# Optimization experiments

Hardware: AMD Instinct MI355X
Metric: run time of the kernel (lower is better)

## Reference

```python
import jax, jax.numpy as jnp
import numpy as np
from jax import lax

L, B, N, D = 6, 4, 2048, 512
H, DH = 8, 64
ID = H * DH           # 512
M = 266               # int(64*log(64)) random features
INNER = 2 * D         # conformer expansion
K = 31                # depthwise kernel
PAD = (15, 15)        # calc_same_padding(31)
EPS_LN = 1e-5


def setup_inputs() -> dict:
    key = jax.random.key(0)
    ks = jax.random.split(key, 12)
    s = 0.02
    return {
        "x": jax.random.normal(ks[0], (B, N, D), jnp.float32),
        "ln1_g": jnp.ones((L, D), jnp.float32),
        "ln1_b": jnp.zeros((L, D), jnp.float32),
        "wq": jax.random.normal(ks[1], (L, ID, D), jnp.float32) * s,
        "bq": jnp.zeros((L, ID), jnp.float32),
        "wk": jax.random.normal(ks[2], (L, ID, D), jnp.float32) * s,
        "bk": jnp.zeros((L, ID), jnp.float32),
        "wv": jax.random.normal(ks[3], (L, ID, D), jnp.float32) * s,
        "bv": jnp.zeros((L, ID), jnp.float32),
        "wo": jax.random.normal(ks[4], (L, ID, D), jnp.float32) * s,
        "bo": jnp.zeros((L, D), jnp.float32),
        # FAVOR+ random projection buffer (gaussian orthogonal ~ iid gaussian rows)
        "proj": jax.random.normal(ks[5], (L, M, DH), jnp.float32),
        "ln2_g": jnp.ones((L, D), jnp.float32),
        "ln2_b": jnp.zeros((L, D), jnp.float32),
        "pw1_w": jax.random.normal(ks[6], (L, 2 * INNER, D), jnp.float32) * s,
        "pw1_b": jnp.zeros((L, 2 * INNER), jnp.float32),
        "dw_w": jax.random.normal(ks[7], (L, INNER, K), jnp.float32) * s,
        "dw_b": jnp.zeros((L, INNER), jnp.float32),
        "pw2_w": jax.random.normal(ks[8], (L, D, INNER), jnp.float32) * s,
        "pw2_b": jnp.zeros((L, D), jnp.float32),
    }


def layer_norm(x, g, b):
    mu = jnp.mean(x, axis=-1, keepdims=True)
    var = jnp.mean((x - mu) ** 2, axis=-1, keepdims=True)
    return (x - mu) * lax.rsqrt(var + EPS_LN) * g + b


def softmax_kernel(data, proj, is_query, eps=1e-4):
    # data: [b,h,n,dh], proj: [m,dh]
    dn = DH ** -0.25
    ratio = M ** -0.5
    data_dash = jnp.einsum('bhnd,md->bhnm', dn * data, proj)
    diag = jnp.sum(data * data, axis=-1, keepdims=True) * 0.5 * dn * dn  # [b,h,n,1]
    if is_query:
        mx = jnp.max(data_dash, axis=-1, keepdims=True)
        return ratio * (jnp.exp(data_dash - diag - mx) + eps)
    else:
        return ratio * jnp.exp(data_dash - diag + eps)


def favor_attention(q, k, v, proj):
    qp = softmax_kernel(q, proj, True)   # [b,h,n,m]
    kp = softmax_kernel(k, proj, False)  # [b,h,n,m]
    k_cumsum = jnp.sum(kp, axis=-2)      # [b,h,m]
    d_inv = 1.0 / (jnp.einsum('bhnm,bhm->bhn', qp, k_cumsum) + 1e-8)
    context = jnp.einsum('bhnm,bhne->bhme', kp, v)          # [b,h,m,dh]
    out = jnp.einsum('bhme,bhnm,bhn->bhne', context, qp, d_inv)
    return out


def pcmer_forward(x, ln1_g, ln1_b, wq, bq, wk, bk, wv, bv, wo, bo, proj,
                  ln2_g, ln2_b, pw1_w, pw1_b, dw_w, dw_b, pw2_w, pw2_b):
    for l in range(L):
        # --- self attention (FAVOR+) ---
        h = layer_norm(x, ln1_g[l], ln1_b[l])
        q = (h @ wq[l].T + bq[l]).reshape(B, N, H, DH).transpose(0, 2, 1, 3)
        k = (h @ wk[l].T + bk[l]).reshape(B, N, H, DH).transpose(0, 2, 1, 3)
        v = (h @ wv[l].T + bv[l]).reshape(B, N, H, DH).transpose(0, 2, 1, 3)
        o = favor_attention(q, k, v, proj[l])                 # [b,h,n,dh]
        o = o.transpose(0, 2, 1, 3).reshape(B, N, ID)
        x = x + (o @ wo[l].T + bo[l])
        # --- conformer conv module ---
        h = layer_norm(x, ln2_g[l], ln2_b[l])
        y = h @ pw1_w[l].T + pw1_b[l]                         # [b,n,2*inner]
        a, g = y[..., :INNER], y[..., INNER:]
        y = a * jax.nn.sigmoid(g)                             # GLU
        yt = jnp.pad(y.transpose(0, 2, 1), ((0, 0), (0, 0), PAD))  # [b,inner,n+30]
        dw = lax.conv_general_dilated(
            yt, dw_w[l][:, None, :], window_strides=(1,), padding='VALID',
            feature_group_count=INNER,
            dimension_numbers=('NCH', 'OIH', 'NCH')) + dw_b[l][None, :, None]
        dw = jax.nn.silu(dw).transpose(0, 2, 1)               # [b,n,inner]
        x = x + (dw @ pw2_w[l].T + pw2_b[l])
    return x


def reference(x, ln1_g, ln1_b, wq, bq, wk, bk, wv, bv, wo, bo, proj,
              ln2_g, ln2_b, pw1_w, pw1_b, dw_w, dw_b, pw2_w, pw2_b):
    return pcmer_forward(x, ln1_g, ln1_b, wq, bq, wk, bk, wv, bv, wo, bo, proj,
                         ln2_g, ln2_b, pw1_w, pw1_b, dw_w, dw_b, pw2_w, pw2_b)
```

## Files before the change

### kernel.cpp

```cpp
#include <hip/hip_runtime.h>


#define L_LAYERS 6
#define B_ 4
#define N_ 2048
#define D_ 512
#define H_ 8
#define DH_ 64
#define M_ 266
#define INNER_ 1024
#define T_ 8192
#define PS_ 320
#define QKVS_ 1536
#define NS_ 8

typedef __attribute__((ext_vector_type(8))) short short8;
typedef __attribute__((ext_vector_type(4))) float floatx4;

__device__ __forceinline__ ushort f2bf(float f) {
  union { float f; uint u; } v; v.f = f;
  uint r = v.u + 0x7fffu + ((v.u >> 16) & 1u);
  return (ushort)(r >> 16);
}
__device__ __forceinline__ float bf2f(ushort u) {
  union { uint u; float f; } v; v.u = ((uint)u) << 16;
  return v.f;
}
__device__ __forceinline__ float wave_sum(float v) {
#pragma unroll
  for (int m = 1; m < 64; m <<= 1) v += __shfl_xor(v, m);
  return v;
}
__device__ __forceinline__ void async_cp16(const void* g, void* l) {
  __builtin_amdgcn_global_load_lds(
      (const __attribute__((address_space(1))) void*)g,
      (__attribute__((address_space(3))) void*)l, 16, 0, 0);
}
__device__ __forceinline__ int xcd_swz(int bid, int n) {
  return (bid & 7) * (n >> 3) + (bid >> 3);
}

__global__ void f2bf4_dual(const float4* __restrict__ s1, int n1,
                           const float4* __restrict__ s2, int n2,
                           ushort* __restrict__ out) {
  int i = blockIdx.x * 256 + threadIdx.x;
  if (i >= n1 + n2) return;
  float4 v = (i < n1) ? s1[i] : s2[i - n1];
  ushort4 r;
  r.x = f2bf(v.x); r.y = f2bf(v.y); r.z = f2bf(v.z); r.w = f2bf(v.w);
  *(ushort4*)(out + (size_t)i * 4) = r;
}
__global__ void pack_qkv_w3(const float4* __restrict__ wq, const float4* __restrict__ wk,
                            const float4* __restrict__ wv, ushort* __restrict__ dst) {
  int i = blockIdx.x * 256 + threadIdx.x;
  const int per = L_LAYERS * 512 * 128;
  if (i >= 3 * per) return;
  int seg = i / per;
  int rem = i - seg * per;
  const float4* src = seg == 0 ? wq : (seg == 1 ? wk : wv);
  int l = rem >> 16;
  int r2 = rem & 65535;
  int row = r2 >> 7, c4 = r2 & 127;
  float4 v = src[rem];
  ushort4 r;
  r.x = f2bf(v.x); r.y = f2bf(v.y); r.z = f2bf(v.z); r.w = f2bf(v.w);
  *(ushort4*)(dst + ((size_t)l * QKVS_ + seg * 512 + row) * 512 + c4 * 4) = r;
}
__global__ void pack_small(const float* __restrict__ bq, const float* __restrict__ bk,
                           const float* __restrict__ bv, float* __restrict__ bqkv,
                           const float* __restrict__ proj, ushort* __restrict__ pjp,
                           const float* __restrict__ pw1b, float* __restrict__ pb1) {
  int i = blockIdx.x * 256 + threadIdx.x;
  const int A = L_LAYERS * QKVS_;
  const int Bn = L_LAYERS * 320 * 64;
  const int C = L_LAYERS * 2048;
  if (i < A) {
    int l = i / QKVS_, c = i % QKVS_;
    bqkv[i] = c < 512 ? bq[l * 512 + c]
                      : (c < 1024 ? bk[l * 512 + c - 512] : bv[l * 512 + c - 1024]);
  } else if (i < A + Bn) {
    int j = i - A;
    int l = j / (320 * 64), rem = j % (320 * 64), m = rem >> 6, kk = rem & 63;
    pjp[j] = (m < M_) ? f2bf(proj[((size_t)l * M_ + m) * 64 + kk]) : (ushort)0;
  } else if (i < A + Bn + C) {
    int j = i - A - Bn;
    int l = j >> 11, cp = j & 2047;
    int s = (cp >> 4) & 1;
    int srow = ((cp >> 5) << 4) + (cp & 15) + s * 1024;
    pb1[j] = pw1b[l * 2048 + srow];
  }
}
__global__ void pack_pw1_w(const float4* __restrict__ src, ushort* __restrict__ dst) {
  int i = blockIdx.x * 256 + threadIdx.x;
  if (i >= L_LAYERS * 2048 * 128) return;
  int l = i >> 18;
  int rem = i & 262143;
  int cp = rem >> 7, c4 = rem & 127;
  int s = (cp >> 4) & 1;
  int srow = ((cp >> 5) << 4) + (cp & 15) + s * 1024;
  float4 v = src[((size_t)l * 2048 + srow) * 128 + c4];
  ushort4 r;
  r.x = f2bf(v.x); r.y = f2bf(v.y); r.z = f2bf(v.z); r.w = f2bf(v.w);
  *(ushort4*)(dst + ((size_t)l * 2048 + cp) * 512 + c4 * 4) = r;
}

__global__ __launch_bounds__(256) void ln_kernel(const float* __restrict__ x,
                                                 const float* __restrict__ g,
                                                 const float* __restrict__ b,
                                                 ushort* __restrict__ out) {
  const int t = blockIdx.x;
  const int tid = threadIdx.x;
  const float* row = x + (size_t)t * D_;
  float v0 = row[tid], v1 = row[tid + 256];
  float s1 = v0 + v1;
  float s2 = v0 * v0 + v1 * v1;
  s1 = wave_sum(s1);
  s2 = wave_sum(s2);
  __shared__ float sh1[4], sh2[4];
  int w = tid >> 6;
  if ((tid & 63) == 0) { sh1[w] = s1; sh2[w] = s2; }
  __syncthreads();
  s1 = sh1[0] + sh1[1] + sh1[2] + sh1[3];
  s2 = sh2[0] + sh2[1] + sh2[2] + sh2[3];
  float mu = s1 * (1.f / D_);
  float var = s2 * (1.f / D_) - mu * mu;
  float rs = rsqrtf(var + 1e-5f);
  out[(size_t)t * D_ + tid]       = f2bf((v0 - mu) * rs * g[tid] + b[tid]);
  out[(size_t)t * D_ + tid + 256] = f2bf((v1 - mu) * rs * g[tid + 256] + b[tid + 256]);
}

template <bool OUT_BF16, int ACT, int KT>
__global__ __launch_bounds__(256, 2) void gemm_big(const ushort* __restrict__ A,
                                                   const ushort* __restrict__ W,
                                                   const float* __restrict__ bias,
                                                   void* __restrict__ Cout,
                                                   int ldc) {
  constexpr int NT = KT / 32;
  __shared__ ushort As[3][256 * 32];
  __shared__ ushort Bs[3][128 * 32];
  const int tid = threadIdx.x;
  const int w = tid >> 6, lane = tid & 63;
  const int row0 = xcd_swz(blockIdx.x, gridDim.x) * 256, col0 = blockIdx.y * 128;
  const int rl = lane >> 2;
  const int lc = ((lane & 3) ^ ((lane >> 3) & 3)) * 8;
  const ushort* gA = A + (size_t)(row0 + w * 64 + rl) * KT + lc;
  const ushort* gB = W + (size_t)(col0 + w * 32 + rl) * KT + lc;
  const int m16 = lane & 15, quad = lane >> 4;
  const int awr = (w >> 1) * 128;
  const int bwc = (w & 1) * 64;
  floatx4 acc[8][4] = {};

  auto stage = [&](int t, int buf) {
#pragma unroll
    for (int j = 0; j < 4; j++)
      async_cp16(gA + ((size_t)j * 16) * KT + t * 32, As[buf] + w * 2048 + j * 512);
#pragma unroll
    for (int j = 0; j < 2; j++)
      async_cp16(gB + ((size_t)j * 16) * KT + t * 32, Bs[buf] + w * 1024 + j * 512);
  };
  auto body = [&](int buf, bool bar2) {
    short8 af[8], bfr[4];
#pragma unroll
    for (int i = 0; i < 8; i++) {
      int r = awr + i * 16 + m16;
      af[i] = *(const short8*)&As[buf][r * 32 + (quad ^ ((r >> 1) & 3)) * 8];
    }
#pragma unroll
    for (int j = 0; j < 4; j++) {
      int r = bwc + j * 16 + m16;
      bfr[j] = *(const short8*)&Bs[buf][r * 32 + (quad ^ ((r >> 1) & 3)) * 8];
    }
    if (bar2) {
      asm volatile("s_waitcnt lgkmcnt(0)" ::: "memory");
      __builtin_amdgcn_sched_barrier(0);
      __builtin_amdgcn_s_barrier();
    }
    __builtin_amdgcn_s_setprio(1);
#pragma unroll
    for (int i = 0; i < 8; i++)
#pragma unroll
      for (int j = 0; j < 4; j++)
        acc[i][j] = __builtin_amdgcn_mfma_f32_16x16x32_bf16(af[i], bfr[j], acc[i][j], 0, 0, 0);
    __builtin_amdgcn_s_setprio(0);
  };

  stage(0, 0);
  stage(1, 1);
  int c = 0;
  for (int t = 0; t < NT - 2; t++) {
    int pf = c + 2; if (pf >= 3) pf -= 3;
    stage(t + 2, pf);
    asm volatile("s_waitcnt vmcnt(12)" ::: "memory");
    __builtin_amdgcn_s_barrier();
    body(c, true);
    c++; if (c >= 3) c -= 3;
  }
  asm volatile("s_waitcnt vmcnt(6)" ::: "memory");
  __builtin_amdgcn_s_barrier();
  body(c, false);
  c++; if (c >= 3) c -= 3;
  asm volatile("s_waitcnt vmcnt(0)" ::: "memory");
  __builtin_amdgcn_s_barrier();
  body(c, false);

  if (ACT == 0) {
#pragma unroll
    for (int i = 0; i < 8; i++) {
      const int r0 = row0 + awr + i * 16 + quad * 4;
#pragma unroll
      for (int j = 0; j < 4; j++) {
        const int cc = col0 + bwc + j * 16 + m16;
        const float bv = bias[cc];
#pragma unroll
        for (int r = 0; r < 4; r++) {
          float vv = acc[i][j][r] + bv;
          if (OUT_BF16) ((ushort*)Cout)[(size_t)(r0 + r) * ldc + cc] = f2bf(vv);
          else          ((float*)Cout)[(size_t)(r0 + r) * ldc + cc] = vv;
        }
      }
    }
  } else {
#pragma unroll
    for (int i = 0; i < 8; i++) {
      const int r0 = row0 + awr + i * 16 + quad * 4;
#pragma unroll
      for (int jp = 0; jp < 2; jp++) {
        const int j = jp * 2;
        const int ca = col0 + bwc + j * 16 + m16;
        const float ba = bias[ca], bg = bias[ca + 16];
        const int oc = ((col0 + bwc) >> 1) + jp * 16 + m16;
#pragma unroll
        for (int r = 0; r < 4; r++) {
          float a = acc[i][j][r] + ba;
          float g = acc[i][j + 1][r] + bg;
          float z = a / (1.f + expf(-g));
          ((ushort*)Cout)[(size_t)(r0 + r) * ldc + oc] = f2bf(z);
        }
      }
    }
  }
}

template <int KT>
__global__ __launch_bounds__(256, 4) void gemm_small(const ushort* __restrict__ A,
                                                     const ushort* __restrict__ W,
                                                     const float* __restrict__ bias,
                                                     const float* __restrict__ res,
                                                     float* __restrict__ Cout,
                                                     int ldc) {
  constexpr int NT = KT / 32;
  __shared__ ushort As[3][64 * 32];
  __shared__ ushort Bs[3][128 * 32];
  const int tid = threadIdx.x;
  const int w = tid >> 6, lane = tid & 63;
  const int row0 = xcd_swz(blockIdx.x, gridDim.x) * 64, col0 = blockIdx.y * 128;
  const int rl = lane >> 2;
  const int lc = ((lane & 3) ^ ((lane >> 3) & 3)) * 8;
  const ushort* gA = A + (size_t)(row0 + w * 16 + rl) * KT + lc;
  const ushort* gB0 = W + (size_t)(col0 + w * 32 + rl) * KT + lc;
  const ushort* gB1 = gB0 + (size_t)16 * KT;
  const int m16 = lane & 15, quad = lane >> 4;
  const int awr = (w >> 1) * 32;
  const int bwc = (w & 1) * 64;
  floatx4 acc[2][4] = {};

  auto stage = [&](int t, int buf) {
    async_cp16(gA + t * 32, As[buf] + w * 512);
    async_cp16(gB0 + t * 32, Bs[buf] + w * 1024);
    async_cp16(gB1 + t * 32, Bs[buf] + w * 1024 + 512);
  };
  auto body = [&](int buf, bool bar2) {
    short8 af[2], bfr[4];
#pragma unroll
    for (int i = 0; i < 2; i++) {
      int r = awr + i * 16 + m16;
      af[i] = *(const short8*)&As[buf][r * 32 + (quad ^ ((r >> 1) & 3)) * 8];
    }
#pragma unroll
    for (int j = 0; j < 4; j++) {
      int r = bwc + j * 16 + m16;
      bfr[j] = *(const short8*)&Bs[buf][r * 32 + (quad ^ ((r >> 1) & 3)) * 8];
    }
    if (bar2) {
      asm volatile("s_waitcnt lgkmcnt(0)" ::: "memory");
      __builtin_amdgcn_sched_barrier(0);
      __builtin_amdgcn_s_barrier();
    }
    __builtin_amdgcn_s_setprio(1);
#pragma unroll
    for (int i = 0; i < 2; i++)
#pragma unroll
      for (int j = 0; j < 4; j++)
        acc[i][j] = __builtin_amdgcn_mfma_f32_16x16x32_bf16(af[i], bfr[j], acc[i][j], 0, 0, 0);
    __builtin_amdgcn_s_setprio(0);
  };

  stage(0, 0);
  stage(1, 1);
  int c = 0;
  for (int t = 0; t < NT - 2; t++) {
    int pf = c + 2; if (pf >= 3) pf -= 3;
    stage(t + 2, pf);
    asm volatile("s_waitcnt vmcnt(6)" ::: "memory");
    __builtin_amdgcn_s_barrier();
    body(c, true);
    c++; if (c >= 3) c -= 3;
  }
  asm volatile("s_waitcnt vmcnt(3)" ::: "memory");
  __builtin_amdgcn_s_barrier();
  body(c, false);
  c++; if (c >= 3) c -= 3;
  asm volatile("s_waitcnt vmcnt(0)" ::: "memory");
  __builtin_amdgcn_s_barrier();
  body(c, false);

#pragma unroll
  for (int i = 0; i < 2; i++) {
    const int r0 = row0 + awr + i * 16 + quad * 4;
#pragma unroll
    for (int j = 0; j < 4; j++) {
      const int cc = col0 + bwc + j * 16 + m16;
      const float bv = bias[cc];
#pragma unroll
      for (int r = 0; r < 4; r++)
        Cout[(size_t)(r0 + r) * ldc + cc] =
            acc[i][j][r] + bv + res[(size_t)(r0 + r) * ldc + cc];
    }
  }
}

__global__ __launch_bounds__(256) void ctx_phi_mfma(const ushort* __restrict__ qkv,
                                                    const ushort* __restrict__ projp,
                                                    float* __restrict__ part,
                                                    float* __restrict__ kpart) {
  __shared__ ushort projs[64 * 64];
  __shared__ ushort kts[32 * 64];
  __shared__ ushort kps[64][40];
  __shared__ ushort vsT[64][40];
  __shared__ float diag_sh[32];
  __shared__ float kshare[4][64];
  const int bh = xcd_swz(blockIdx.x, 32), mt = blockIdx.y, ns = blockIdx.z;
  const int b = bh >> 3, h = bh & 7;
  const int m0 = mt * 64;
  const int tid = threadIdx.x;
  const int w = tid >> 6, lane = tid & 63, l16 = lane & 15, quad = lane >> 4;
  const int rl8 = lane >> 3;
  const int lc8 = ((lane & 7) ^ (rl8 & 7)) * 8;
#pragma unroll
  for (int j = 0; j < 2; j++) {
    const int rb = w * 16 + j * 8;
    async_cp16(projp + (size_t)(m0 + rb + rl8) * 64 + lc8, projs + rb * 64);
  }
  const int nn = tid >> 3;
  const int a8 = tid & 7;
  const int gn = nn >> 3, jn = nn & 7;
  const int pc = ((gn ^ (a8 & 3)) << 3) | jn;
  const int km = tid & 63, kg = tid >> 6;
  const float dn = 0.35355339059327373f;
  const float ratio = 0.06131393394849658f;
  floatx4 acc[4] = {};
  float ksp = 0.f;
  for (int nstep = 0; nstep < 2048 / NS_ / 32; nstep++) {
    const int n0 = ns * (2048 / NS_) + nstep * 32;
    {
      const int rb = w * 8;
      async_cp16(qkv + (size_t)(b * N_ + n0 + rb + rl8) * QKVS_ + 512 + h * 64 + lc8,
                 kts + rb * 64);
    }
    uint4 vv = *(const uint4*)(qkv + ((size_t)(b * N_ + n0 + nn)) * QKVS_ + 1024 + h * 64 + a8 * 8);
    __syncthreads();
    {
      const int r = tid >> 3;
      const int c = tid & 7;
      short8 kv8 = *(const short8*)&kts[r * 64 + c * 8];
      const ushort* u = (const ushort*)&kv8;
      float s = 0.f;
#pragma unroll
      for (int j = 0; j < 8; j++) { float f = bf2f(u[j]); s += f * f; }
      s += __shfl_xor(s, 1);
      s += __shfl_xor(s, 2);
      s += __shfl_xor(s, 4);
      if ((tid & 7) == 0) diag_sh[r] = 0.0625f * s;
    }
    {
      const ushort* ve = (const ushort*)&vv;
#pragma unroll
      for (int j = 0; j < 8; j++) vsT[a8 * 8 + j][pc] = ve[j];
    }
    __syncthreads();
    floatx4 pacc[2] = {};
    __builtin_amdgcn_s_setprio(1);
#pragma unroll
    for (int s = 0; s < 2; s++) {
      const int ar = w * 16 + l16;
      short8 af = *(const short8*)&projs[ar * 64 + ((s * 4 + quad) ^ (ar & 7)) * 8];
#pragma unroll
      for (int nj = 0; nj < 2; nj++) {
        const int br = nj * 16 + l16;
        short8 bf = *(const short8*)&kts[br * 64 + ((s * 4 + quad) ^ (br & 7)) * 8];
        pacc[nj] = __builtin_amdgcn_mfma_f32_16x16x32_bf16(af, bf, pacc[nj], 0, 0, 0);
      }
    }
    __builtin_amdgcn_s_setprio(0);
#pragma unroll
    for (int nj = 0; nj < 2; nj++) {
      const int n = nj * 16 + l16;
      const float dgn = diag_sh[n];
#pragma unroll
      for (int r = 0; r < 4; r++) {
        const int m = w * 16 + quad * 4 + r;
        float val = (m0 + m < M_) ? ratio * expf(dn * pacc[nj][r] - dgn + 1e-4f) : 0.f;
        kps[m][(((n >> 3) ^ ((m >> 3) & 3)) << 3) | (n & 7)] = f2bf(val);
      }
    }
    __syncthreads();
    const int am = w * 16 + l16;
    const int apg = quad ^ ((am >> 3) & 3);
    short8 af = *(const short8*)&kps[am][apg * 8];
    __builtin_amdgcn_s_setprio(1);
#pragma unroll
    for (int et = 0; et < 4; et++) {
      const int be = et * 16 + l16;
      const int bpg = quad ^ ((be >> 3) & 3);
      short8 bf = *(const short8*)&vsT[be][bpg * 8];
      acc[et] = __builtin_amdgcn_mfma_f32_16x16x32_bf16(af, bf, acc[et], 0, 0, 0);
    }
    __builtin_amdgcn_s_setprio(0);
    {
      short8 kr = *(const short8*)&kps[km][kg * 8];
      const ushort* ku = (const ushort*)&kr;
#pragma unroll
      for (int j = 0; j < 8; j++) ksp += bf2f(ku[j]);
    }
  }
  float* pb = part + ((size_t)(bh * NS_ + ns) * 5 + mt) * 4096;
#pragma unroll
  for (int et = 0; et < 4; et++)
#pragma unroll
    for (int r = 0; r < 4; r++)
      pb[(w * 16 + quad * 4 + r) * 64 + et * 16 + l16] = acc[et][r];
  kshare[kg][km] = ksp;
  __syncthreads();
  if (tid < 64)
    kpart[((size_t)(bh * NS_ + ns) * 5 + mt) * 64 + tid] =
        kshare[0][tid] + kshare[1][tid] + kshare[2][tid] + kshare[3][tid];
}

__global__ __launch_bounds__(256) void ctx_reduce(const float* __restrict__ part,
                                                  const float* __restrict__ kpart,
                                                  ushort* __restrict__ ctxbT,
                                                  float* __restrict__ ksum) {
  const int bh = blockIdx.x, mt = blockIdx.y;
  const int tid = threadIdx.x;
  const int w = tid >> 6, lane = tid & 63;
  for (int oc = w; oc < 8; oc += 4) {
    const int mbase = mt * 64 + oc * 8;
    if (mbase < 288) {
      float s[8] = {0.f, 0.f, 0.f, 0.f, 0.f, 0.f, 0.f, 0.f};
#pragma unroll
      for (int ns = 0; ns < NS_; ns++) {
        const float* pb = part + ((size_t)(bh * NS_ + ns) * 5 + mt) * 4096;
#pragma unroll
        for (int ml = 0; ml < 8; ml++) s[ml] += pb[(oc * 8 + ml) * 64 + lane];
      }
      ushort tmp[8];
#pragma unroll
      for (int ml = 0; ml < 8; ml++) tmp[ml] = f2bf(s[ml]);
      *(short8*)(ctxbT + ((size_t)(bh * 64 + lane)) * 288 + mbase) = *(const short8*)tmp;
    }
  }
  if (tid < 64) {
    float s = 0.f;
#pragma unroll
    for (int ns = 0; ns < NS_; ns++)
      s += kpart[((size_t)(bh * NS_ + ns) * 5 + mt) * 64 + tid];
    ksum[(size_t)bh * PS_ + mt * 64 + tid] = s;
  }
}

__global__ __launch_bounds__(256, 4) void attn_fused(const ushort* __restrict__ qkv,
                                                     const ushort* __restrict__ projp,
                                                     const ushort* __restrict__ ctxbT,
                                                     const float* __restrict__ ksum,
                                                     ushort* __restrict__ o) {
  __shared__ __align__(16) ushort sm[14336];
  __shared__ float ks_sh[288];
  __shared__ float diag_sh[64];
  ushort* As = sm;
  ushort* Bs = sm + 4096;
  ushort (*qst)[40] = (ushort(*)[40])sm;
  const int bh = xcd_swz(blockIdx.x, 32), b = bh >> 3, h = bh & 7;
  const int n0 = blockIdx.y * 64;
  const int tid = threadIdx.x;
  const int w = tid >> 6, lane = tid & 63, l16 = lane & 15, quad = lane >> 4;
  const int rl8 = lane >> 3;
  const int lc8 = ((lane & 7) ^ (rl8 & 7)) * 8;
#pragma unroll
  for (int j = 0; j < 2; j++) {
    const int rb = w * 16 + j * 8;
    async_cp16(qkv + (size_t)(b * N_ + n0 + rb + rl8) * QKVS_ + h * 64 + lc8, As + rb * 64);
  }
#pragma unroll
  for (int j = 0; j < 5; j++) {
    const int rb = w * 40 + j * 8;
    async_cp16(projp + (size_t)(rb + rl8) * 64 + lc8, Bs + rb * 64);
  }
  for (int i = tid; i < 288; i += 256) ks_sh[i] = ksum[(size_t)bh * PS_ + i];
  __syncthreads();
  {
    const int r = w * 16 + (lane >> 2);
    const int c0 = 2 * (lane & 3);
    float s = 0.f;
#pragma unroll
    for (int cc = 0; cc < 2; cc++) {
      short8 vv = *(const short8*)&As[r * 64 + ((c0 + cc) ^ (r & 7)) * 8];
      const ushort* u = (const ushort*)&vv;
#pragma unroll
      for (int j = 0; j < 8; j++) { float f = bf2f(u[j]); s += f * f; }
    }
    s += __shfl_xor(s, 1);
    s += __shfl_xor(s, 2);
    if ((lane & 3) == 0) diag_sh[r] = 0.0625f * s;
  }
  __syncthreads();
  float dgr[4];
#pragma unroll
  for (int r = 0; r < 4; r++) dgr[r] = diag_sh[w * 16 + quad * 4 + r];
  floatx4 acc[18];
#pragma unroll
  for (int cf = 0; cf < 18; cf++) acc[cf] = (floatx4){0.f, 0.f, 0.f, 0.f};
  const int ar = w * 16 + l16;
  __builtin_amdgcn_s_setprio(1);
#pragma unroll
  for (int s = 0; s < 2; s++) {
    short8 af = *(const short8*)&As[ar * 64 + ((s * 4 + quad) ^ (ar & 7)) * 8];
#pragma unroll
    for (int cf = 0; cf < 10; cf++) {
      const int br = cf * 16 + l16;
      short8 bf = *(const short8*)&Bs[br * 64 + ((s * 4 + quad) ^ (br & 7)) * 8];
      acc[cf] = __builtin_amdgcn_mfma_f32_16x16x32_bf16(af, bf, acc[cf], 0, 0, 0);
    }
  }
  __builtin_amdgcn_s_setprio(0);
  __syncthreads();
#pragma unroll
  for (int j = 0; j < 4; j++) {
    const int rb = w * 32 + j * 8;
    async_cp16(projp + (size_t)(160 + rb + rl8) * 64 + lc8, Bs + rb * 64);
  }
  __syncthreads();
  __builtin_amdgcn_s_setprio(1);
#pragma unroll
  for (int s = 0; s < 2; s++) {
    short8 af = *(const short8*)&As[ar * 64 + ((s * 4 + quad) ^ (ar & 7)) * 8];
#pragma unroll
    for (int cf = 10; cf < 18; cf++) {
      const int br = (cf - 10) * 16 + l16;
      short8 bf = *(const short8*)&Bs[br * 64 + ((s * 4 + quad) ^ (br & 7)) * 8];
      acc[cf] = __builtin_amdgcn_mfma_f32_16x16x32_bf16(af, bf, acc[cf], 0, 0, 0);
    }
  }
  __builtin_amdgcn_s_setprio(0);
  const float dn = 0.35355339059327373f;
  const float ratio = 0.06131393394849658f;
  float mxr[4];
#pragma unroll
  for (int r = 0; r < 4; r++) {
    float mx = -1e30f;
#pragma unroll
    for (int cf = 0; cf < 18; cf++) {
      const int col = cf * 16 + l16;
      if (col < M_) mx = fmaxf(mx, dn * acc[cf][r]);
    }
    mx = fmaxf(mx, __shfl_xor(mx, 1));
    mx = fmaxf(mx, __shfl_xor(mx, 2));
    mx = fmaxf(mx, __shfl_xor(mx, 4));
    mx = fmaxf(mx, __shfl_xor(mx, 8));
    mxr[r] = mx;
  }
  __syncthreads();
  float dacc[4] = {0.f, 0.f, 0.f, 0.f};
  floatx4 acc2[4] = {};
  const ushort* ctxrow = ctxbT + (size_t)bh * (64 * 288);
  for (int m0 = 0; m0 < 288; m0 += 32) {
    const int cf0 = m0 >> 4;
#pragma unroll
    for (int cc = 0; cc < 2; cc++) {
      const int col = m0 + cc * 16 + l16;
      const float kv = ks_sh[col];
#pragma unroll
      for (int r = 0; r < 4; r++) {
        float val = (col < M_) ? ratio * (expf(dn * acc[cf0 + cc][r] - dgr[r] - mxr[r]) + 1e-4f)
                               : 0.f;
        qst[w * 16 + quad * 4 + r][cc * 16 + l16] = f2bf(val);
        dacc[r] += val * kv;
      }
    }
    short8 af = *(const short8*)&qst[w * 16 + l16][quad * 8];
    __builtin_amdgcn_s_setprio(1);
#pragma unroll
    for (int et = 0; et < 4; et++) {
      short8 bf = *(const short8*)(ctxrow + (size_t)(et * 16 + l16) * 288 + m0 + quad * 8);
      acc2[et] = __builtin_amdgcn_mfma_f32_16x16x32_bf16(af, bf, acc2[et], 0, 0, 0);
    }
    __builtin_amdgcn_s_setprio(0);
  }
  float di[4];
#pragma unroll
  for (int r = 0; r < 4; r++) {
    float d = dacc[r];
    d += __shfl_xor(d, 1);
    d += __shfl_xor(d, 2);
    d += __shfl_xor(d, 4);
    d += __shfl_xor(d, 8);
    di[r] = 1.f / (d + 1e-8f);
  }
#pragma unroll
  for (int r = 0; r < 4; r++) {
    const int n = n0 + w * 16 + quad * 4 + r;
#pragma unroll
    for (int et = 0; et < 4; et++)
      o[((size_t)(b * N_ + n)) * 512 + h * 64 + et * 16 + l16] = f2bf(acc2[et][r] * di[r]);
  }
}

#define TN_ 32
__global__ __launch_bounds__(256) void dwconv_kernel(const ushort* __restrict__ x,
                                                     const float* __restrict__ w,
                                                     const float* __restrict__ bias,
                                                     ushort* __restrict__ out) {
  const int bid = blockIdx.x;
  const int cb = bid & 3;
  const int nb = (bid >> 2) & (N_ / TN_ - 1);
  const int b  = bid >> 8;
  const int c = cb * 256 + threadIdx.x;
  const int n0 = nb * TN_;
  float win[TN_ + 30];
#pragma unroll
  for (int i = 0; i < TN_ + 30; i++) {
    int nn = n0 + i - 15;
    win[i] = (nn >= 0 && nn < N_) ? bf2f(x[(size_t)(b * N_ + nn) * INNER_ + c]) : 0.f;
  }
  float wc[31];
#pragma unroll
  for (int kk = 0; kk < 31; kk++) wc[kk] = w[c * 31 + kk];
  const float bsv = bias[c];
#pragma unroll
  for (int j = 0; j < TN_; j++) {
    float acc = bsv;
#pragma unroll
    for (int kk = 0; kk < 31; kk++) acc += win[j + kk] * wc[kk];
    acc = acc / (1.f + expf(-acc));
    out[(size_t)(b * N_ + n0 + j) * INNER_ + c] = f2bf(acc);
  }
}

extern "C" void kernel_launch(void* const* d_in, const int* in_sizes, int n_in,
                              void* d_out, int out_size, void* d_ws, size_t ws_size,
                              hipStream_t stream) {
  const float* in_x  = (const float*)d_in[0];
  const float* ln1_g = (const float*)d_in[1];
  const float* ln1_b = (const float*)d_in[2];
  const float* wq    = (const float*)d_in[3];
  const float* bq    = (const float*)d_in[4];
  const float* wk    = (const float*)d_in[5];
  const float* bk    = (const float*)d_in[6];
  const float* wv    = (const float*)d_in[7];
  const float* bv    = (const float*)d_in[8];
  const float* wo    = (const float*)d_in[9];
  const float* bo    = (const float*)d_in[10];
  const float* proj  = (const float*)d_in[11];
  const float* ln2_g = (const float*)d_in[12];
  const float* ln2_b = (const float*)d_in[13];
  const float* pw1_w = (const float*)d_in[14];
  const float* pw1_b = (const float*)d_in[15];
  const float* dw_w  = (const float*)d_in[16];
  const float* dw_b  = (const float*)d_in[17];
  const float* pw2_w = (const float*)d_in[18];
  const float* pw2_b = (const float*)d_in[19];

  char* cur = (char*)d_ws;
  auto alloc = [&](size_t bytes) { char* p = cur; cur += (bytes + 255) & ~(size_t)255; return p; };
  float*  x    = (float*)alloc((size_t)T_ * D_ * 4);
  ushort* p    = (ushort*)alloc((size_t)T_ * INNER_ * 2 * 2);
  float*  part = (float*)alloc((size_t)32 * NS_ * 5 * 4096 * 4);
  float*  kpart= (float*)alloc((size_t)32 * NS_ * 5 * 64 * 4);
  ushort* ctxb = (ushort*)alloc((size_t)32 * 288 * 64 * 2);
  float*  ksum = (float*)alloc((size_t)32 * PS_ * 4);
  ushort* h    = (ushort*)alloc((size_t)T_ * D_ * 2);
  ushort* qkv  = (ushort*)alloc((size_t)T_ * QKVS_ * 2);
  ushort* obuf = (ushort*)alloc((size_t)T_ * D_ * 2);
  ushort* wqkv_b = (ushort*)alloc((size_t)L_LAYERS * QKVS_ * 512 * 2);
  float*  bqkv   = (float*)alloc((size_t)L_LAYERS * QKVS_ * 4);
  ushort* wo_b = (ushort*)alloc((size_t)L_LAYERS * D_ * D_ * 2 + (size_t)L_LAYERS * D_ * INNER_ * 2);
  ushort* p2_b = wo_b + (size_t)L_LAYERS * D_ * D_;
  ushort* pjp  = (ushort*)alloc((size_t)L_LAYERS * 320 * 64 * 2);
  ushort* p1_b = (ushort*)alloc((size_t)L_LAYERS * 2048 * D_ * 2);
  float*  pb1  = (float*)alloc((size_t)L_LAYERS * 2048 * 4);
  ushort* glu  = p;
  ushort* conv = p + (size_t)T_ * INNER_;

  pack_qkv_w3<<<(3 * L_LAYERS * 512 * 128 + 255) / 256, 256, 0, stream>>>(
      (const float4*)wq, (const float4*)wk, (const float4*)wv, wqkv_b);
  pack_pw1_w<<<(L_LAYERS * 2048 * 128 + 255) / 256, 256, 0, stream>>>((const float4*)pw1_w, p1_b);
  {
    int n1 = L_LAYERS * D_ * D_ / 4;
    int n2 = L_LAYERS * D_ * INNER_ / 4;
    f2bf4_dual<<<(n1 + n2 + 255) / 256, 256, 0, stream>>>(
        (const float4*)wo, n1, (const float4*)pw2_w, n2, wo_b);
  }
  {
    int tot = L_LAYERS * QKVS_ + L_LAYERS * 320 * 64 + L_LAYERS * 2048;
    pack_small<<<(tot + 255) / 256, 256, 0, stream>>>(bq, bk, bv, bqkv, proj, pjp, pw1_b, pb1);
  }

  for (int l = 0; l < L_LAYERS; l++) {
    const ushort* wqkvl = wqkv_b + (size_t)l * QKVS_ * 512;
    const ushort* wol = wo_b + (size_t)l * D_ * D_;
    const ushort* pjl = pjp + (size_t)l * 320 * 64;
    const ushort* p1l = p1_b + (size_t)l * 2048 * D_;
    const ushort* p2l = p2_b + (size_t)l * D_ * INNER_;
    const float*  dwl = dw_w + (size_t)l * INNER_ * 31;
    const float*  dwbl = dw_b + (size_t)l * INNER_;
    const float*  xin = (l == 0) ? in_x : x;
    float* xout = (l == L_LAYERS - 1) ? (float*)d_out : x;

    ln_kernel<<<T_, 256, 0, stream>>>(xin, ln1_g + l * D_, ln1_b + l * D_, h);
    gemm_big<true, 0, 512><<<dim3(T_ / 256, QKVS_ / 128), 256, 0, stream>>>(
        h, wqkvl, bqkv + (size_t)l * QKVS_, qkv, QKVS_);
    ctx_phi_mfma<<<dim3(32, 5, NS_), 256, 0, stream>>>(qkv, pjl, part, kpart);
    ctx_reduce<<<dim3(32, 5), 256, 0, stream>>>(part, kpart, ctxb, ksum);
    attn_fused<<<dim3(32, 32), 256, 0, stream>>>(qkv, pjl, ctxb, ksum, obuf);
    gemm_small<512><<<dim3(T_ / 64, 4), 256, 0, stream>>>(
        obuf, wol, bo + l * D_, xin, x, D_);
    ln_kernel<<<T_, 256, 0, stream>>>(x, ln2_g + l * D_, ln2_b + l * D_, h);
    gemm_big<true, 1, 512><<<dim3(T_ / 256, 16), 256, 0, stream>>>(
        h, p1l, pb1 + (size_t)l * 2048, glu, INNER_);
    dwconv_kernel<<<B_ * (N_ / TN_) * 4, 256, 0, stream>>>(glu, dwl, dwbl, conv);
    gemm_small<1024><<<dim3(T_ / 64, 4), 256, 0, stream>>>(
        conv, p2l, pw2_b + l * D_, x, xout, D_);
  }
}
```

Before: 1.249 ms.

## Replace small GEMM with 128x128 tile kernel, drop XCD swizzle and setprio, use fast exp

```diff
diff --git a/kernel.cpp b/kernel.cpp
--- a/kernel.cpp
+++ b/kernel.cpp
@@ -35,9 +35,6 @@
   __builtin_amdgcn_global_load_lds(
       (const __attribute__((address_space(1))) void*)g,
       (__attribute__((address_space(3))) void*)l, 16, 0, 0);
-}
-__device__ __forceinline__ int xcd_swz(int bid, int n) {
-  return (bid & 7) * (n >> 3) + (bid >> 3);
 }
 
 __global__ void f2bf4_dual(const float4* __restrict__ s1, int n1,
@@ -129,6 +126,117 @@
   out[(size_t)t * D_ + tid + 256] = f2bf((v1 - mu) * rs * g[tid + 256] + b[tid + 256]);
 }
 
+template <bool HAS_RES, bool OUT_BF16, int ACT, int KT>
+__global__ __launch_bounds__(256) void gemm_mfma(const ushort* __restrict__ A,
+                                                 const ushort* __restrict__ W,
+                                                 const float* __restrict__ bias,
+                                                 const float* __restrict__ res,
+                                                 void* __restrict__ Cout,
+                                                 int ldc) {
+  constexpr int NT = KT / 32;
+  __shared__ ushort As[3][128 * 32];
+  __shared__ ushort Bs[3][128 * 32];
+  const int tid = threadIdx.x;
+  const int w = tid >> 6, lane = tid & 63;
+  const int row0 = blockIdx.x * 128, col0 = blockIdx.y * 128;
+  const int rl = lane >> 2;
+  const int lc = ((lane & 3) ^ ((lane >> 3) & 3)) * 8;
+  const ushort* gA0 = A + (size_t)(row0 + w * 32 + rl) * KT + lc;
+  const ushort* gA1 = gA0 + (size_t)16 * KT;
+  const ushort* gB0 = W + (size_t)(col0 + w * 32 + rl) * KT + lc;
+  const ushort* gB1 = gB0 + (size_t)16 * KT;
+  const int m16 = lane & 15, quad = lane >> 4;
+  const int awr = (w >> 1) * 64, bwc = (w & 1) * 64;
+  floatx4 acc[4][4] = {};
+
+  auto stage = [&](int t, int buf) {
+    async_cp16(gA0 + t * 32, As[buf] + w * 1024);
+    async_cp16(gA1 + t * 32, As[buf] + w * 1024 + 512);
+    async_cp16(gB0 + t * 32, Bs[buf] + w * 1024);
+    async_cp16(gB1 + t * 32, Bs[buf] + w * 1024 + 512);
+  };
+  auto body = [&](int buf, bool bar2) {
+    short8 af[4], bfr[4];
+#pragma unroll
+    for (int i = 0; i < 4; i++) {
+      int r = awr + i * 16 + m16;
+      af[i] = *(const short8*)&As[buf][r * 32 + (quad ^ ((r >> 1) & 3)) * 8];
+    }
+#pragma unroll
+    for (int j = 0; j < 4; j++) {
+      int r = bwc + j * 16 + m16;
+      bfr[j] = *(const short8*)&Bs[buf][r * 32 + (quad ^ ((r >> 1) & 3)) * 8];
+    }
+    if (bar2) {
+      asm volatile("s_waitcnt lgkmcnt(0)" ::: "memory");
+      __builtin_amdgcn_sched_barrier(0);
+      __builtin_amdgcn_s_barrier();
+    }
+#pragma unroll
+    for (int i = 0; i < 4; i++)
+#pragma unroll
+      for (int j = 0; j < 4; j++)
+        acc[i][j] = __builtin_amdgcn_mfma_f32_16x16x32_bf16(af[i], bfr[j], acc[i][j], 0, 0, 0);
+  };
+
+  stage(0, 0);
+  stage(1, 1);
+  int c = 0;
+  for (int t = 0; t < NT - 2; t++) {
+    int pf = c + 2; if (pf >= 3) pf -= 3;
+    stage(t + 2, pf);
+    asm volatile("s_waitcnt vmcnt(8)" ::: "memory");
+    __builtin_amdgcn_s_barrier();
+    body(c, true);
+    c++; if (c >= 3) c -= 3;
+  }
+  asm volatile("s_waitcnt vmcnt(4)" ::: "memory");
+  __builtin_amdgcn_s_barrier();
+  body(c, false);
+  c++; if (c >= 3) c -= 3;
+  asm volatile("s_waitcnt vmcnt(0)" ::: "memory");
+  __builtin_amdgcn_s_barrier();
+  body(c, false);
+
+  if (ACT == 0) {
+#pragma unroll
+    for (int i = 0; i < 4; i++) {
+      const int r0 = row0 + awr + i * 16 + quad * 4;
+#pragma unroll
+      for (int j = 0; j < 4; j++) {
+        const int cc = col0 + bwc + j * 16 + m16;
+        const float bv = bias[cc];
+#pragma unroll
+        for (int r = 0; r < 4; r++) {
+          float vv = acc[i][j][r] + bv;
+          if (HAS_RES) vv += res[(size_t)(r0 + r) * ldc + cc];
+          if (OUT_BF16) ((ushort*)Cout)[(size_t)(r0 + r) * ldc + cc] = f2bf(vv);
+          else          ((float*)Cout)[(size_t)(r0 + r) * ldc + cc] = vv;
+        }
+      }
+    }
+  } else {
+#pragma unroll
+    for (int i = 0; i < 4; i++) {
+      const int r0 = row0 + awr + i * 16 + quad * 4;
+#pragma unroll
+      for (int jp = 0; jp < 2; jp++) {
+        const int j = jp * 2;
+        const int ca = col0 + bwc + j * 16 + m16;
+        const float ba = bias[ca], bg = bias[ca + 16];
+        const int oc = ((col0 + bwc) >> 1) + jp * 16 + m16;
+#pragma unroll
+        for (int r = 0; r < 4; r++) {
+          float a = acc[i][j][r] + ba;
+          float g = acc[i][j + 1][r] + bg;
+          float z = a / (1.f + __expf(-g));
+          ((ushort*)Cout)[(size_t)(r0 + r) * ldc + oc] = f2bf(z);
+        }
+      }
+    }
+  }
+}
+
 template <bool OUT_BF16, int ACT, int KT>
 __global__ __launch_bounds__(256, 2) void gemm_big(const ushort* __restrict__ A,
                                                    const ushort* __restrict__ W,
@@ -140,7 +248,7 @@
   __shared__ ushort Bs[3][128 * 32];
   const int tid = threadIdx.x;
   const int w = tid >> 6, lane = tid & 63;
-  const int row0 = xcd_swz(blockIdx.x, gridDim.x) * 256, col0 = blockIdx.y * 128;
+  const int row0 = blockIdx.x * 256, col0 = blockIdx.y * 128;
   const int rl = lane >> 2;
   const int lc = ((lane & 3) ^ ((lane >> 3) & 3)) * 8;
   const ushort* gA = A + (size_t)(row0 + w * 64 + rl) * KT + lc;
@@ -175,13 +283,11 @@
       __builtin_amdgcn_sched_barrier(0);
       __builtin_amdgcn_s_barrier();
     }
-    __builtin_amdgcn_s_setprio(1);
 #pragma unroll
     for (int i = 0; i < 8; i++)
 #pragma unroll
       for (int j = 0; j < 4; j++)
         acc[i][j] = __builtin_amdgcn_mfma_f32_16x16x32_bf16(af[i], bfr[j], acc[i][j], 0, 0, 0);
-    __builtin_amdgcn_s_setprio(0);
   };
 
   stage(0, 0);
@@ -233,98 +339,10 @@
         for (int r = 0; r < 4; r++) {
           float a = acc[i][j][r] + ba;
           float g = acc[i][j + 1][r] + bg;
-          float z = a / (1.f + expf(-g));
+          float z = a / (1.f + __expf(-g));
           ((ushort*)Cout)[(size_t)(r0 + r) * ldc + oc] = f2bf(z);
         }
       }
-    }
-  }
-}
-
-template <int KT>
-__global__ __launch_bounds__(256, 4) void gemm_small(const ushort* __restrict__ A,
-                                                     const ushort* __restrict__ W,
-                                                     const float* __restrict__ bias,
-                                                     const float* __restrict__ res,
-                                                     float* __restrict__ Cout,
-                                                     int ldc) {
-  constexpr int NT = KT / 32;
-  __shared__ ushort As[3][64 * 32];
-  __shared__ ushort Bs[3][128 * 32];
-  const int tid = threadIdx.x;
-  const int w = tid >> 6, lane = tid & 63;
-  const int row0 = xcd_swz(blockIdx.x, gridDim.x) * 64, col0 = blockIdx.y * 128;
-  const int rl = lane >> 2;
-  const int lc = ((lane & 3) ^ ((lane >> 3) & 3)) * 8;
-  const ushort* gA = A + (size_t)(row0 + w * 16 + rl) * KT + lc;
-  const ushort* gB0 = W + (size_t)(col0 + w * 32 + rl) * KT + lc;
-  const ushort* gB1 = gB0 + (size_t)16 * KT;
-  const int m16 = lane & 15, quad = lane >> 4;
-  const int awr = (w >> 1) * 32;
-  const int bwc = (w & 1) * 64;
-  floatx4 acc[2][4] = {};
-
-  auto stage = [&](int t, int buf) {
-    async_cp16(gA + t * 32, As[buf] + w * 512);
-    async_cp16(gB0 + t * 32, Bs[buf] + w * 1024);
-    async_cp16(gB1 + t * 32, Bs[buf] + w * 1024 + 512);
-  };
-  auto body = [&](int buf, bool bar2) {
-    short8 af[2], bfr[4];
-#pragma unroll
-    for (int i = 0; i < 2; i++) {
-      int r = awr + i * 16 + m16;
-      af[i] = *(const short8*)&As[buf][r * 32 + (quad ^ ((r >> 1) & 3)) * 8];
-    }
-#pragma unroll
-    for (int j = 0; j < 4; j++) {
-      int r = bwc + j * 16 + m16;
-      bfr[j] = *(const short8*)&Bs[buf][r * 32 + (quad ^ ((r >> 1) & 3)) * 8];
-    }
-    if (bar2) {
-      asm volatile("s_waitcnt lgkmcnt(0)" ::: "memory");
-      __builtin_amdgcn_sched_barrier(0);
-      __builtin_amdgcn_s_barrier();
-    }
-    __builtin_amdgcn_s_setprio(1);
-#pragma unroll
-    for (int i = 0; i < 2; i++)
-#pragma unroll
-      for (int j = 0; j < 4; j++)
-        acc[i][j] = __builtin_amdgcn_mfma_f32_16x16x32_bf16(af[i], bfr[j], acc[i][j], 0, 0, 0);
-    __builtin_amdgcn_s_setprio(0);
-  };
-
-  stage(0, 0);
-  stage(1, 1);
-  int c = 0;
-  for (int t = 0; t < NT - 2; t++) {
-    int pf = c + 2; if (pf >= 3) pf -= 3;
-    stage(t + 2, pf);
-    asm volatile("s_waitcnt vmcnt(6)" ::: "memory");
-    __builtin_amdgcn_s_barrier();
-    body(c, true);
-    c++; if (c >= 3) c -= 3;
-  }
-  asm volatile("s_waitcnt vmcnt(3)" ::: "memory");
-  __builtin_amdgcn_s_barrier();
-  body(c, false);
-  c++; if (c >= 3) c -= 3;
-  asm volatile("s_waitcnt vmcnt(0)" ::: "memory");
-  __builtin_amdgcn_s_barrier();
-  body(c, false);
-
-#pragma unroll
-  for (int i = 0; i < 2; i++) {
-    const int r0 = row0 + awr + i * 16 + quad * 4;
-#pragma unroll
-    for (int j = 0; j < 4; j++) {
-      const int cc = col0 + bwc + j * 16 + m16;
-      const float bv = bias[cc];
-#pragma unroll
-      for (int r = 0; r < 4; r++)
-        Cout[(size_t)(r0 + r) * ldc + cc] =
-            acc[i][j][r] + bv + res[(size_t)(r0 + r) * ldc + cc];
     }
   }
 }
@@ -339,7 +357,7 @@
   __shared__ ushort vsT[64][40];
   __shared__ float diag_sh[32];
   __shared__ float kshare[4][64];
-  const int bh = xcd_swz(blockIdx.x, 32), mt = blockIdx.y, ns = blockIdx.z;
+  const int bh = blockIdx.x, mt = blockIdx.y, ns = blockIdx.z;
   const int b = bh >> 3, h = bh & 7;
   const int m0 = mt * 64;
   const int tid = threadIdx.x;
@@ -409,7 +427,7 @@
 #pragma unroll
       for (int r = 0; r < 4; r++) {
         const int m = w * 16 + quad * 4 + r;
-        float val = (m0 + m < M_) ? ratio * expf(dn * pacc[nj][r] - dgn + 1e-4f) : 0.f;
+        float val = (m0 + m < M_) ? ratio * __expf(dn * pacc[nj][r] - dgn + 1e-4f) : 0.f;
         kps[m][(((n >> 3) ^ ((m >> 3) & 3)) << 3) | (n & 7)] = f2bf(val);
       }
     }
@@ -489,7 +507,7 @@
   ushort* As = sm;
   ushort* Bs = sm + 4096;
   ushort (*qst)[40] = (ushort(*)[40])sm;
-  const int bh = xcd_swz(blockIdx.x, 32), b = bh >> 3, h = bh & 7;
+  const int bh = blockIdx.x, b = bh >> 3, h = bh & 7;
   const int n0 = blockIdx.y * 64;
   const int tid = threadIdx.x;
   const int w = tid >> 6, lane = tid & 63, l16 = lane & 15, quad = lane >> 4;
@@ -590,7 +608,7 @@
       const float kv = ks_sh[col];
 #pragma unroll
       for (int r = 0; r < 4; r++) {
-        float val = (col < M_) ? ratio * (expf(dn * acc[cf0 + cc][r] - dgr[r] - mxr[r]) + 1e-4f)
+        float val = (col < M_) ? ratio * (__expf(dn * acc[cf0 + cc][r] - dgr[r] - mxr[r]) + 1e-4f)
                                : 0.f;
         qst[w * 16 + quad * 4 + r][cc * 16 + l16] = f2bf(val);
         dacc[r] += val * kv;
@@ -650,7 +668,7 @@
     float acc = bsv;
 #pragma unroll
     for (int kk = 0; kk < 31; kk++) acc += win[j + kk] * wc[kk];
-    acc = acc / (1.f + expf(-acc));
+    acc = acc / (1.f + __expf(-acc));
     out[(size_t)(b * N_ + n0 + j) * INNER_ + c] = f2bf(acc);
   }
 }
@@ -731,13 +749,13 @@
     ctx_phi_mfma<<<dim3(32, 5, NS_), 256, 0, stream>>>(qkv, pjl, part, kpart);
     ctx_reduce<<<dim3(32, 5), 256, 0, stream>>>(part, kpart, ctxb, ksum);
     attn_fused<<<dim3(32, 32), 256, 0, stream>>>(qkv, pjl, ctxb, ksum, obuf);
-    gemm_small<512><<<dim3(T_ / 64, 4), 256, 0, stream>>>(
+    gemm_mfma<true, false, 0, 512><<<dim3(T_ / 128, 4), 256, 0, stream>>>(
         obuf, wol, bo + l * D_, xin, x, D_);
     ln_kernel<<<T_, 256, 0, stream>>>(x, ln2_g + l * D_, ln2_b + l * D_, h);
     gemm_big<true, 1, 512><<<dim3(T_ / 256, 16), 256, 0, stream>>>(
         h, p1l, pb1 + (size_t)l * 2048, glu, INNER_);
     dwconv_kernel<<<B_ * (N_ / TN_) * 4, 256, 0, stream>>>(glu, dwl, dwbl, conv);
-    gemm_small<1024><<<dim3(T_ / 64, 4), 256, 0, stream>>>(
+    gemm_mfma<true, false, 0, 1024><<<dim3(T_ / 128, 4), 256, 0, stream>>>(
         conv, p2l, pw2_b + l * D_, x, xout, D_);
   }
 }
```

After: 1.189 ms. 4.9% less time.
